# Performance work log

Measured on AMD Instinct MI355X. Metric: run time of the kernel, lower is better.

Reference implementation:

```python
import jax, jax.numpy as jnp
import numpy as np

B, N, C, H, D, K = 8, 2000, 64, 64, 16, 2  # batch, nodes, hidden, hidden_hidden, embed_dim, cheb_k


def setup_inputs() -> dict:
    key = jax.random.key(0)
    ks = jax.random.split(key, 12)
    f = lambda k, s, sc=1.0: jax.random.normal(k, s, dtype=jnp.float32) * sc
    return {
        "z": f(ks[0], (B, N, C)),
        "W_in": f(ks[1], (H, C), 0.1),
        "b_in": f(ks[2], (H,), 0.1),
        "W_out": f(ks[3], (C * C, H), 0.05),
        "b_out": f(ks[4], (C * C,), 0.05),
        "emb": f(ks[5], (N, D), 0.1),
        "wp": f(ks[6], (D, K, H, H), 0.1),
        "bp": f(ks[7], (D, H), 0.1),
        "w1": f(ks[8], (C,)),
        "w2": f(ks[9], (C,)),
        "vs": f(ks[10], (N, N), 0.02),
        "bs": f(ks[11], (N, N), 0.02),
    }


def reference(z, W_in, b_in, W_out, b_out, emb, wp, bp, w1, w2, vs, bs):
    # linear_in + relu: (B,N,C) -> (B,N,H)
    h = jax.nn.relu(jnp.einsum("bnc,hc->bnh", z, W_in) + b_in)

    # data-adaptive graph: softmax over rows of relu(emb @ emb^T)
    A = jax.nn.softmax(jax.nn.relu(emb @ emb.T), axis=1)  # (N,N)
    S = jnp.stack([jnp.eye(N, dtype=z.dtype), A], axis=0)  # (K,N,N), cheb_k=2

    # spatial attention on h (x = h.unsqueeze(1), f_in == H == C)
    e1 = h @ w1  # (B,N)
    e2 = h @ w2  # (B,N)
    prod = e1[:, :, None] * e2[:, None, :]  # (B,N,N) outer product
    E = jax.nn.softmax(
        jnp.einsum("nm,bmp->bnp", vs, jax.nn.sigmoid(prod + bs)), axis=-1
    )  # (B,N,N)

    # batched supports: E.unsqueeze(1) @ S -> (B,K,N,N)
    sup = jnp.einsum("bnm,kmp->bknp", E, S)

    # node-adaptive weights / bias
    weights = jnp.einsum("nd,dkio->nkio", emb, wp)  # (N,K,H,H)
    bias = emb @ bp  # (N,H)

    # graph conv
    x_g = jnp.einsum("bknm,bmc->bnkc", sup, h)  # (B,N,K,H)
    g = jnp.einsum("bnki,nkio->bno", x_g, weights) + bias  # (B,N,H)

    # linear_out + view + tanh, scaled by 0.1
    out = jnp.tanh(jnp.einsum("bnh,oh->bno", g, W_out) + b_out)
    return 0.1 * out.reshape(B, N, C, C)
```

## Files before the change

### kernel.cpp

```cpp
#include <hip/hip_runtime.h>
#include <hip/hip_bf16.h>

#define NN 2000
#define NP 2048
#define BB 8
#define HH 64
#define DD 16

typedef __hip_bfloat16 bf16;
typedef short bf16x8 __attribute__((ext_vector_type(8)));
typedef float f32x4 __attribute__((ext_vector_type(4)));

__device__ __forceinline__ float fast_sigmoid(float x) {
    return 1.0f / (1.0f + __expf(-x));
}
__device__ __forceinline__ float fast_tanh(float x) {
    float e = __expf(2.0f * x);
    return 1.0f - 2.0f / (e + 1.0f);
}

__device__ __forceinline__ void glds16(const void* g, void* l) {
    __builtin_amdgcn_global_load_lds(
        (const __attribute__((address_space(1))) void*)g,
        (__attribute__((address_space(3))) void*)l, 16, 0, 0);
}

__global__ __launch_bounds__(256) void k_h(
        const float* __restrict__ z, const float* __restrict__ W_in,
        const float* __restrict__ b_in, const float* __restrict__ w1,
        const float* __restrict__ w2, float* __restrict__ h,
        float* __restrict__ e1, float* __restrict__ e2) {
    __shared__ float WT[64 * 65];
    __shared__ float zs[4][64];
    int t = threadIdx.x;
    int lane = t & 63, ty = t >> 6;
    int bn0 = blockIdx.x * 4;
    for (int i = t; i < 64 * 64; i += 256) {
        int hh = i >> 6, c = i & 63;
        WT[c * 65 + hh] = W_in[i];
    }
    zs[ty][lane] = z[(size_t)(bn0 + ty) * 64 + lane];
    __syncthreads();
    float acc = b_in[lane];
    #pragma unroll
    for (int c = 0; c < 64; c++) acc += zs[ty][c] * WT[c * 65 + lane];
    float hv = fmaxf(acc, 0.0f);
    h[(size_t)(bn0 + ty) * 64 + lane] = hv;
    float p1 = hv * w1[lane], p2 = hv * w2[lane];
    #pragma unroll
    for (int off = 32; off > 0; off >>= 1) {
        p1 += __shfl_down(p1, off);
        p2 += __shfl_down(p2, off);
    }
    if (lane == 0) { e1[bn0 + ty] = p1; e2[bn0 + ty] = p2; }
}

__global__ __launch_bounds__(256) void k_A(const float* __restrict__ emb,
                                           bf16* __restrict__ A) {
    int i = blockIdx.x, t = threadIdx.x;
    if (i >= NN) {
        for (int j = t; j < NP; j += 256) A[(size_t)i * NP + j] = __float2bfloat16(0.0f);
        return;
    }
    __shared__ float ei[DD];
    __shared__ float rowbuf[NP];
    __shared__ float red[256];
    if (t < DD) ei[t] = emb[i * DD + t];
    __syncthreads();
    float lmax = -1e30f;
    for (int j = t; j < NP; j += 256) {
        float s = 0.0f;
        if (j < NN) {
            #pragma unroll
            for (int d = 0; d < DD; d++) s += ei[d] * emb[j * DD + d];
            s = fmaxf(s, 0.0f);
            lmax = fmaxf(lmax, s);
        }
        rowbuf[j] = s;
    }
    red[t] = lmax; __syncthreads();
    for (int o = 128; o > 0; o >>= 1) { if (t < o) red[t] = fmaxf(red[t], red[t + o]); __syncthreads(); }
    float mx = red[0];
    __syncthreads();
    float lsum = 0.0f;
    for (int j = t; j < NN; j += 256) {
        float e = __expf(rowbuf[j] - mx);
        rowbuf[j] = e; lsum += e;
    }
    red[t] = lsum; __syncthreads();
    for (int o = 128; o > 0; o >>= 1) { if (t < o) red[t] += red[t + o]; __syncthreads(); }
    float inv = 1.0f / red[0];
    for (int j = t; j < NP; j += 256)
        A[(size_t)i * NP + j] = __float2bfloat16(j < NN ? rowbuf[j] * inv : 0.0f);
}

__global__ __launch_bounds__(256) void k_misc(
        const float* __restrict__ vs, bf16* __restrict__ vs_bf,
        const float* __restrict__ W_out, bf16* __restrict__ Wo_bf,
        const float* __restrict__ emb, const float* __restrict__ wp,
        float* __restrict__ Wn_all) {
    __shared__ float embs[128 * 16];
    int bid = blockIdx.x, t = threadIdx.x;
    if (bid < 16384) {
        int id = bid * 256 + t;
        int n = id >> 11, m = id & (NP - 1);
        float v = (n < NN && m < NN) ? vs[n * NN + m] : 0.0f;
        vs_bf[id] = __float2bfloat16(v);
        return;
    }
    if (bid < 16384 + 1024) {
        int id = (bid - 16384) * 256 + t;
        Wo_bf[id] = __float2bfloat16(W_out[id]);
        return;
    }
    int wb = bid - 17408;
    int n0 = (wb & 15) * 128;
    int jo = (wb >> 4) * 256 + t;
    float wv[16];
    #pragma unroll
    for (int d = 0; d < 16; d++) wv[d] = wp[(size_t)d * 8192 + jo];
    for (int s = t; s < 128 * 16; s += 256) {
        int i = s >> 4, d = s & 15;
        int n = n0 + i;
        embs[s] = (n < NN) ? emb[n * 16 + d] : 0.f;
    }
    __syncthreads();
    for (int i = 0; i < 128; i++) {
        int n = n0 + i;
        if (n >= NN) break;
        const f32x4* ev = (const f32x4*)&embs[i * 16];
        f32x4 e0 = ev[0], e1 = ev[1], e2 = ev[2], e3 = ev[3];
        float a = 0.f;
        #pragma unroll
        for (int q = 0; q < 4; q++) a += e0[q] * wv[q];
        #pragma unroll
        for (int q = 0; q < 4; q++) a += e1[q] * wv[4 + q];
        #pragma unroll
        for (int q = 0; q < 4; q++) a += e2[q] * wv[8 + q];
        #pragma unroll
        for (int q = 0; q < 4; q++) a += e3[q] * wv[12 + q];
        Wn_all[(size_t)n * 8192 + jo] = a;
    }
}

__global__ __launch_bounds__(256) void k_hT(const float* __restrict__ h,
                                            bf16* __restrict__ hTcat,
                                            bf16* __restrict__ hsT) {
    __shared__ float tile[64 * 65];
    int nt = blockIdx.x, b = blockIdx.y;
    int tx = threadIdx.x & 63, ty = threadIdx.x >> 6;
    int n0 = nt * 64;
    for (int i = ty * 16; i < ty * 16 + 16; i++) {
        int n = n0 + i;
        tile[i * 65 + tx] = (n < NN) ? h[((size_t)b * NN + n) * 64 + tx] : 0.0f;
    }
    __syncthreads();
    for (int i = ty * 16; i < ty * 16 + 16; i++) {
        bf16 v = __float2bfloat16(tile[tx * 65 + i]);
        hTcat[((size_t)b * 64 + i) * NP + n0 + tx] = v;
        hsT[((size_t)b * 128 + i) * NP + n0 + tx] = v;
    }
}

__global__ __launch_bounds__(256) void k_AhT(const float* __restrict__ Ahcat,
                                             bf16* __restrict__ hsT) {
    __shared__ float tile[64 * 65];
    int pt = blockIdx.x, b = blockIdx.y;
    int tx = threadIdx.x & 63, ty = threadIdx.x >> 6;
    int p0 = pt * 64, q0 = b * 64;
    for (int i = ty * 16; i < ty * 16 + 16; i++)
        tile[i * 65 + tx] = Ahcat[((size_t)p0 + i) * 512 + q0 + tx];
    __syncthreads();
    for (int i = ty * 16; i < ty * 16 + 16; i++)
        hsT[((size_t)b * 128 + 64 + i) * NP + p0 + tx] =
            __float2bfloat16(tile[tx * 65 + i]);
}

__global__ __launch_bounds__(256) void k_Tt(const float* __restrict__ e1,
                                            const float* __restrict__ e2,
                                            const float* __restrict__ bs,
                                            bf16* __restrict__ Tt) {
    __shared__ float bst[64 * 65];
    __shared__ float tile[64 * 65];
    int mt = blockIdx.x, pt = blockIdx.y;
    int tx = threadIdx.x & 63, ty = threadIdx.x >> 6;
    int m0 = mt * 64, p0 = pt * 64;
    int p = p0 + tx;
    for (int i = ty * 16; i < ty * 16 + 16; i++) {
        int m = m0 + i;
        bst[i * 65 + tx] = (m < NN && p < NN) ? bs[(size_t)m * NN + p] : 0.0f;
    }
    __syncthreads();
    for (int b = 0; b < BB; b++) {
        float e2v = (p < NN) ? e2[b * NN + p] : 0.0f;
        for (int i = ty * 16; i < ty * 16 + 16; i++) {
            int m = m0 + i;
            float v = 0.0f;
            if (m < NN && p < NN)
                v = fast_sigmoid(e1[b * NN + m] * e2v + bst[i * 65 + tx]);
            tile[i * 65 + tx] = v;
        }
        __syncthreads();
        for (int i = ty * 16; i < ty * 16 + 16; i++)
            Tt[(size_t)b * NP * NP + ((size_t)p0 + i) * NP + m0 + tx] =
                __float2bfloat16(tile[tx * 65 + i]);
        __syncthreads();
    }
}

__global__ __launch_bounds__(512) void k_gemm256pv(
        const bf16* __restrict__ X, const bf16* __restrict__ Yt,
        const bf16* __restrict__ hsT, float* __restrict__ xgPart,
        float* __restrict__ rsPart,
        int K, int ldx, int ldy, long long sY, long long sHs) {
    __shared__ short LDSb[65536];
    short* Asb = LDSb;
    short* Bsb = LDSb + 32768;
    int id = blockIdx.x;
    int xcd = id & 7, jj0 = id >> 3;
    int member = jj0 & 7, glocal = jj0 >> 3;
    int group = glocal * 8 + xcd;
    int bx = member, by = group & 7, bz = group >> 3;
    int z = bz;
    const bf16* Xp = X;
    const bf16* Yp = Yt + (long long)z * sY;
    int tid = threadIdx.x;
    int m0 = bx * 256, n0 = by * 256;
    int wave = tid >> 6, lane = tid & 63;
    int wr = wave >> 2, wc = wave & 3;
    int fr = lane & 15, kq = lane >> 4;

    f32x4 zero = {0.f, 0.f, 0.f, 0.f};
    f32x4 acc[8][4];
    #pragma unroll
    for (int i = 0; i < 8; i++)
        #pragma unroll
        for (int j = 0; j < 4; j++) acc[i][j] = zero;

    int r8 = tid >> 3;
    int sslot = (tid & 7) ^ (r8 & 7);
    const bf16* xsrc = Xp + (long long)(m0 + r8) * ldx + sslot * 8;
    const bf16* ysrc = Yp + (long long)(n0 + r8) * ldy + sslot * 8;

    auto STAGE = [&](int tile) {
        short* Ab = Asb + (tile & 1) * 16384 + tid * 8;
        short* Bb = Bsb + (tile & 1) * 16384 + tid * 8;
        int ko = tile * 64;
        #pragma unroll
        for (int c = 0; c < 4; c++) {
            glds16(xsrc + (long long)(c * 64) * ldx + ko, Ab + c * 4096);
            glds16(ysrc + (long long)(c * 64) * ldy + ko, Bb + c * 4096);
        }
    };

    int NT = K >> 6;
    STAGE(0);
    STAGE(1);
    asm volatile("s_waitcnt vmcnt(8)" ::: "memory");
    __builtin_amdgcn_s_barrier();

    for (int t = 0; t < NT; t++) {
        const short* Ab = Asb + (t & 1) * 16384 + wr * 8192 + fr * 64;
        const short* Bb = Bsb + (t & 1) * 16384 + wc * 4096 + fr * 64;
        #pragma unroll
        for (int ks = 0; ks < 2; ks++) {
            int s = ((ks * 4 + kq) ^ (fr & 7)) * 8;
            bf16x8 a[8], b[4];
            #pragma unroll
            for (int i = 0; i < 8; i++)
                a[i] = *(const bf16x8*)(Ab + i * 1024 + s);
            #pragma unroll
            for (int j = 0; j < 4; j++)
                b[j] = *(const bf16x8*)(Bb + j * 1024 + s);
            __builtin_amdgcn_s_setprio(1);
            #pragma unroll
            for (int i = 0; i < 8; i++)
                #pragma unroll
                for (int j = 0; j < 4; j++)
                    acc[i][j] = __builtin_amdgcn_mfma_f32_16x16x32_bf16(a[i], b[j], acc[i][j], 0, 0, 0);
            __builtin_amdgcn_s_setprio(0);
        }
        __builtin_amdgcn_sched_barrier(0);
        __builtin_amdgcn_s_barrier();
        __builtin_amdgcn_sched_barrier(0);
        if (t + 2 < NT) {
            STAGE(t + 2);
            asm volatile("s_waitcnt vmcnt(8)" ::: "memory");
            __builtin_amdgcn_s_barrier();
        } else if (t + 1 < NT) {
            asm volatile("s_waitcnt vmcnt(0)" ::: "memory");
            __builtin_amdgcn_s_barrier();
        }
    }
    __syncthreads();

    int rq = kq * 4;
    #pragma unroll
    for (int i = 0; i < 8; i++) {
        #pragma unroll
        for (int r = 0; r < 4; r++) {
            int lrow = wr * 128 + i * 16 + rq + r;
            float rs = 0.f;
            #pragma unroll
            for (int j = 0; j < 4; j++) {
                int lcol = wc * 64 + j * 16 + fr;
                float e = (n0 + lcol < NN) ? __expf(acc[i][j][r]) : 0.f;
                bf16 bv = __float2bfloat16(e);
                int sl = (lcol >> 3) ^ (lrow & 7);
                LDSb[lrow * 256 + sl * 8 + (lcol & 7)] = *(short*)&bv;
                rs += e;
            }
            rs += __shfl_xor(rs, 1);
            rs += __shfl_xor(rs, 2);
            rs += __shfl_xor(rs, 4);
            rs += __shfl_xor(rs, 8);
            if (fr == 0)
                rsPart[((long long)z * 32 + by * 4 + wc) * NP + m0 + lrow] = rs;
        }
    }
    __syncthreads();

    const bf16* hz = hsT + (long long)z * sHs;
    int wr2 = wave >> 2, wc2 = wave & 3;
    f32x4 acc2[8][2];
    #pragma unroll
    for (int i = 0; i < 8; i++)
        #pragma unroll
        for (int jj = 0; jj < 2; jj++) acc2[i][jj] = zero;
    #pragma unroll
    for (int ks = 0; ks < 8; ks++) {
        bf16x8 a2[8], b2[2];
        #pragma unroll
        for (int i = 0; i < 8; i++) {
            int row = wr2 * 128 + i * 16 + fr;
            int sl = (ks * 4 + kq) ^ (row & 7);
            a2[i] = *(const bf16x8*)(LDSb + row * 256 + sl * 8);
        }
        #pragma unroll
        for (int jj = 0; jj < 2; jj++)
            b2[jj] = *(const bf16x8*)(hz + (long long)(wc2 * 32 + jj * 16 + fr) * NP
                                      + n0 + ks * 32 + kq * 8);
        #pragma unroll
        for (int i = 0; i < 8; i++)
            #pragma unroll
            for (int jj = 0; jj < 2; jj++)
                acc2[i][jj] = __builtin_amdgcn_mfma_f32_16x16x32_bf16(a2[i], b2[jj], acc2[i][jj], 0, 0, 0);
    }
    long long slab = (long long)by * ((long long)BB * NP * 128);
    #pragma unroll
    for (int i = 0; i < 8; i++)
        #pragma unroll
        for (int jj = 0; jj < 2; jj++) {
            int jcol = wc2 * 32 + jj * 16 + fr;
            #pragma unroll
            for (int r = 0; r < 4; r++) {
                int n = m0 + wr2 * 128 + i * 16 + rq + r;
                xgPart[slab + ((long long)z * NP + n) * 128 + jcol] = acc2[i][jj][r];
            }
        }
}

template<bool TANH, int KSPLIT>
__global__ __launch_bounds__(256) void k_gemm_bt(
        const bf16* __restrict__ X, const bf16* __restrict__ Yt,
        float* __restrict__ C, const float* __restrict__ bias,
        int K, int ldx, int ldy, int ldc,
        long long sX, long long sY, long long sC, long long sSlice) {
    __shared__ short As[128 * 32];
    __shared__ short Bs[128 * 32];
    int zz = blockIdx.z;
    int ks = 0;
    if (KSPLIT > 1) { ks = zz % KSPLIT; zz /= KSPLIT; }
    const bf16* Xp = X + (long long)zz * sX;
    const bf16* Yp = Yt + (long long)zz * sY;
    float* Cp = C + (long long)zz * sC + (long long)ks * sSlice;
    int tid = threadIdx.x;
    int m0 = blockIdx.x * 128, n0 = blockIdx.y * 128;
    int wave = tid >> 6, lane = tid & 63;
    int wm = (wave >> 1) * 64, wn = (wave & 1) * 64;
    int fr = lane & 15, kq = lane >> 4;

    f32x4 zero = {0.f, 0.f, 0.f, 0.f};
    f32x4 acc[4][4];
    #pragma unroll
    for (int i = 0; i < 4; i++)
        #pragma unroll
        for (int j = 0; j < 4; j++) acc[i][j] = zero;

    int lrow = lane >> 2, lcol = (lane & 3) * 8;
    const bf16* xg0 = Xp + (long long)(m0 + wave * 16 + lrow) * ldx + lcol;
    const bf16* xg1 = xg0 + (long long)64 * ldx;
    const bf16* yg0 = Yp + (long long)(n0 + wave * 16 + lrow) * ldy + lcol;
    const bf16* yg1 = yg0 + (long long)64 * ldy;
    short* lA0 = As + wave * 512;
    short* lA1 = As + (wave + 4) * 512;
    short* lB0 = Bs + wave * 512;
    short* lB1 = Bs + (wave + 4) * 512;

    int kbeg = (KSPLIT > 1) ? ks * (K / KSPLIT) : 0;
    int kend = kbeg + K / KSPLIT;
    for (int k0 = kbeg; k0 < kend; k0 += 32) {
        __syncthreads();
        glds16(xg0 + k0, lA0);
        glds16(xg1 + k0, lA1);
        glds16(yg0 + k0, lB0);
        glds16(yg1 + k0, lB1);
        __syncthreads();
        bf16x8 a[4], b[4];
        #pragma unroll
        for (int i = 0; i < 4; i++)
            a[i] = *(const bf16x8*)(As + (wm + i * 16 + fr) * 32 + kq * 8);
        #pragma unroll
        for (int j = 0; j < 4; j++)
            b[j] = *(const bf16x8*)(Bs + (wn + j * 16 + fr) * 32 + kq * 8);
        #pragma unroll
        for (int i = 0; i < 4; i++)
            #pragma unroll
            for (int j = 0; j < 4; j++)
                acc[i][j] = __builtin_amdgcn_mfma_f32_16x16x32_bf16(a[i], b[j], acc[i][j], 0, 0, 0);
    }
    int rq = kq * 4;
    for (int i = 0; i < 4; i++)
        for (int j = 0; j < 4; j++) {
            int col = n0 + wn + j * 16 + fr;
            float bv = TANH ? bias[col] : 0.0f;
            #pragma unroll
            for (int r = 0; r < 4; r++) {
                int row = m0 + wm + i * 16 + rq + r;
                float v = acc[i][j][r];
                Cp[(long long)row * ldc + col] =
                    TANH ? 0.1f * fast_tanh(v + bv) : v;
            }
        }
}

__global__ __launch_bounds__(256) void k_reduce8(const float* __restrict__ part,
                                                 float* __restrict__ out, int total) {
    int i = (blockIdx.x * 256 + threadIdx.x) * 4;
    f32x4 s = *(const f32x4*)(part + i);
    #pragma unroll
    for (int k = 1; k < 8; k++)
        s += *(const f32x4*)(part + (size_t)k * total + i);
    *(f32x4*)(out + i) = s;
}

__global__ __launch_bounds__(256) void k_g(
        const float* __restrict__ Wn_all, const float* __restrict__ bp,
        const float* __restrict__ emb, const float* __restrict__ xgPart,
        const float* __restrict__ rsPart, bf16* __restrict__ gbf) {
    __shared__ float Wn[8192];
    __shared__ float xgs[1024];
    __shared__ float biass[64];
    __shared__ float invs[8];
    const long long TOT = (long long)BB * NP * 128;
    int n = blockIdx.x, t = threadIdx.x;
    if (t < 8) {
        float s = 0.f;
        #pragma unroll
        for (int y = 0; y < 32; y++)
            s += rsPart[((size_t)t * 32 + y) * NP + n];
        invs[t] = 1.0f / s;
    }
    if (t >= 64 && t < 128) {
        int o = t - 64;
        float a = 0.f;
        #pragma unroll
        for (int d = 0; d < 16; d++) a += emb[n * 16 + d] * bp[d * 64 + o];
        biass[o] = a;
    }
    {
        const f32x4* src = (const f32x4*)(Wn_all + (size_t)n * 8192);
        f32x4* dst = (f32x4*)Wn;
        #pragma unroll
        for (int s = 0; s < 8; s++) dst[s * 256 + t] = src[s * 256 + t];
    }
    __syncthreads();
    for (int s = 0; s < 4; s++) {
        int id = t + s * 256;
        int b = id >> 7, j = id & 127;
        long long base = ((long long)b * NP + n) * 128 + j;
        float a = 0.f;
        #pragma unroll
        for (int sl = 0; sl < 8; sl++) a += xgPart[sl * TOT + base];
        xgs[id] = a * invs[b];
    }
    __syncthreads();
    int o = t & 63, bh = t >> 6;
    for (int half = 0; half < 2; half++) {
        int b = bh + half * 4;
        float a = biass[o];
        for (int j = 0; j < 128; j++) a += xgs[b * 128 + j] * Wn[j * 64 + o];
        gbf[((size_t)b * NN + n) * 64 + o] = __float2bfloat16(a);
    }
}

extern "C" void kernel_launch(void* const* d_in, const int* in_sizes, int n_in,
                              void* d_out, int out_size, void* d_ws, size_t ws_size,
                              hipStream_t stream) {
    const float* z     = (const float*)d_in[0];
    const float* W_in  = (const float*)d_in[1];
    const float* b_in  = (const float*)d_in[2];
    const float* W_out = (const float*)d_in[3];
    const float* b_out = (const float*)d_in[4];
    const float* emb   = (const float*)d_in[5];
    const float* wp    = (const float*)d_in[6];
    const float* bp    = (const float*)d_in[7];
    const float* w1    = (const float*)d_in[8];
    const float* w2    = (const float*)d_in[9];
    const float* vs    = (const float*)d_in[10];
    const float* bs    = (const float*)d_in[11];

    char* p = (char*)d_ws;
    auto alloc = [&](size_t bytes) -> char* {
        char* r = p;
        p += (bytes + 255) & ~(size_t)255;
        return r;
    };
    float* h       = (float*)alloc((size_t)BB * NN * 64 * 4);
    float* e1      = (float*)alloc((size_t)BB * NN * 4);
    float* e2      = (float*)alloc((size_t)BB * NN * 4);
    bf16*  A_bf    = (bf16*) alloc((size_t)NP * NP * 2);
    bf16*  vs_bf   = (bf16*) alloc((size_t)NP * NP * 2);
    bf16*  Tt_all  = (bf16*) alloc((size_t)BB * NP * NP * 2);
    float* rsPart  = (float*)alloc((size_t)BB * 32 * NP * 4);
    bf16*  hTcat   = (bf16*) alloc((size_t)512 * NP * 2);
    float* Ahcat   = (float*)alloc((size_t)NP * 512 * 4);
    float* AhPart  = (float*)alloc((size_t)8 * NP * 512 * 4);
    bf16*  hsT     = (bf16*) alloc((size_t)BB * 128 * NP * 2);
    float* xgPart8 = (float*)alloc((size_t)8 * BB * NP * 128 * 4);
    bf16*  gbf     = (bf16*) alloc((size_t)BB * NN * 64 * 2);
    bf16*  Wo_bf   = (bf16*) alloc((size_t)4096 * 64 * 2);
    float* Wn_all  = (float*)alloc((size_t)NN * 8192 * 4);

    k_h<<<BB * NN / 4, 256, 0, stream>>>(z, W_in, b_in, w1, w2, h, e1, e2);
    k_A<<<NP, 256, 0, stream>>>(emb, A_bf);
    k_misc<<<16384 + 1024 + 512, 256, 0, stream>>>(vs, vs_bf, W_out, Wo_bf,
                                                   emb, wp, Wn_all);
    k_hT<<<dim3(NP / 64, BB), 256, 0, stream>>>(h, hTcat, hsT);

    k_gemm_bt<false, 8><<<dim3(16, 4, 8), 256, 0, stream>>>(
        A_bf, hTcat, AhPart, nullptr, NP, NP, NP, 512,
        0, 0, 0, (long long)NP * 512);
    k_reduce8<<<(NP * 512) / 1024, 256, 0, stream>>>(AhPart, Ahcat, NP * 512);
    k_AhT<<<dim3(NP / 64, BB), 256, 0, stream>>>(Ahcat, hsT);

    k_Tt<<<dim3(NP / 64, NP / 64), 256, 0, stream>>>(e1, e2, bs, Tt_all);
    k_gemm256pv<<<512, 512, 0, stream>>>(
        vs_bf, Tt_all, hsT, xgPart8, rsPart, NP, NP, NP,
        (long long)NP * NP, (long long)128 * NP);

    k_g<<<NN, 256, 0, stream>>>(Wn_all, bp, emb, xgPart8, rsPart, gbf);
    k_gemm_bt<true, 1><<<dim3(125, 32, 1), 256, 0, stream>>>(
        gbf, Wo_bf, (float*)d_out, b_out, 64, 64, 64, 4096, 0, 0, 0, 0);
}
```

Baseline: 655.5 us.

## Deepen GEMM pipeline to four K32 stages, fuse reduce into transpose, parallelize Tt over batch

```diff
diff --git a/kernel.cpp b/kernel.cpp
--- a/kernel.cpp
+++ b/kernel.cpp
@@ -162,14 +162,20 @@
     }
 }
 
-__global__ __launch_bounds__(256) void k_AhT(const float* __restrict__ Ahcat,
-                                             bf16* __restrict__ hsT) {
+__global__ __launch_bounds__(256) void k_redT(const float* __restrict__ AhPart,
+                                              bf16* __restrict__ hsT) {
     __shared__ float tile[64 * 65];
     int pt = blockIdx.x, b = blockIdx.y;
     int tx = threadIdx.x & 63, ty = threadIdx.x >> 6;
     int p0 = pt * 64, q0 = b * 64;
-    for (int i = ty * 16; i < ty * 16 + 16; i++)
-        tile[i * 65 + tx] = Ahcat[((size_t)p0 + i) * 512 + q0 + tx];
+    const long long TOT = (long long)NP * 512;
+    for (int i = ty * 16; i < ty * 16 + 16; i++) {
+        long long base = ((long long)p0 + i) * 512 + q0 + tx;
+        float s = AhPart[base];
+        #pragma unroll
+        for (int sl = 1; sl < 8; sl++) s += AhPart[sl * TOT + base];
+        tile[i * 65 + tx] = s;
+    }
     __syncthreads();
     for (int i = ty * 16; i < ty * 16 + 16; i++)
         hsT[((size_t)b * 128 + 64 + i) * NP + p0 + tx] =
@@ -180,32 +186,26 @@
                                             const float* __restrict__ e2,
                                             const float* __restrict__ bs,
                                             bf16* __restrict__ Tt) {
-    __shared__ float bst[64 * 65];
     __shared__ float tile[64 * 65];
+    int b = blockIdx.z;
+    e1 += (size_t)b * NN;
+    e2 += (size_t)b * NN;
+    Tt += (size_t)b * NP * NP;
     int mt = blockIdx.x, pt = blockIdx.y;
     int tx = threadIdx.x & 63, ty = threadIdx.x >> 6;
     int m0 = mt * 64, p0 = pt * 64;
     int p = p0 + tx;
+    float e2v = (p < NN) ? e2[p] : 0.0f;
     for (int i = ty * 16; i < ty * 16 + 16; i++) {
         int m = m0 + i;
-        bst[i * 65 + tx] = (m < NN && p < NN) ? bs[(size_t)m * NN + p] : 0.0f;
-    }
-    __syncthreads();
-    for (int b = 0; b < BB; b++) {
-        float e2v = (p < NN) ? e2[b * NN + p] : 0.0f;
-        for (int i = ty * 16; i < ty * 16 + 16; i++) {
-            int m = m0 + i;
-            float v = 0.0f;
-            if (m < NN && p < NN)
-                v = fast_sigmoid(e1[b * NN + m] * e2v + bst[i * 65 + tx]);
-            tile[i * 65 + tx] = v;
-        }
-        __syncthreads();
-        for (int i = ty * 16; i < ty * 16 + 16; i++)
-            Tt[(size_t)b * NP * NP + ((size_t)p0 + i) * NP + m0 + tx] =
-                __float2bfloat16(tile[tx * 65 + i]);
-        __syncthreads();
-    }
+        float v = 0.0f;
+        if (m < NN && p < NN)
+            v = fast_sigmoid(e1[m] * e2v + bs[(size_t)m * NN + p]);
+        tile[i * 65 + tx] = v;
+    }
+    __syncthreads();
+    for (int i = ty * 16; i < ty * 16 + 16; i++)
+        Tt[((size_t)p0 + i) * NP + m0 + tx] = __float2bfloat16(tile[tx * 65 + i]);
 }
 
 __global__ __launch_bounds__(512) void k_gemm256pv(
@@ -237,60 +237,66 @@
         #pragma unroll
         for (int j = 0; j < 4; j++) acc[i][j] = zero;
 
-    int r8 = tid >> 3;
-    int sslot = (tid & 7) ^ (r8 & 7);
-    const bf16* xsrc = Xp + (long long)(m0 + r8) * ldx + sslot * 8;
-    const bf16* ysrc = Yp + (long long)(n0 + r8) * ldy + sslot * 8;
+    int r4 = tid >> 2, slot = tid & 3;
+    int scol = (slot ^ ((r4 >> 1) & 3)) * 8;
+    const bf16* xsrc = Xp + (long long)(m0 + r4) * ldx + scol;
+    const bf16* ysrc = Yp + (long long)(n0 + r4) * ldy + scol;
+    short* Ad = Asb + tid * 8;
+    short* Bd = Bsb + tid * 8;
 
     auto STAGE = [&](int tile) {
-        short* Ab = Asb + (tile & 1) * 16384 + tid * 8;
-        short* Bb = Bsb + (tile & 1) * 16384 + tid * 8;
-        int ko = tile * 64;
-        #pragma unroll
-        for (int c = 0; c < 4; c++) {
-            glds16(xsrc + (long long)(c * 64) * ldx + ko, Ab + c * 4096);
-            glds16(ysrc + (long long)(c * 64) * ldy + ko, Bb + c * 4096);
-        }
+        int buf = (tile & 3) * 8192;
+        long long ko = (long long)tile * 32;
+        glds16(xsrc + ko, Ad + buf);
+        glds16(xsrc + 128 * (long long)ldx + ko, Ad + buf + 4096);
+        glds16(ysrc + ko, Bd + buf);
+        glds16(ysrc + 128 * (long long)ldy + ko, Bd + buf + 4096);
     };
 
-    int NT = K >> 6;
-    STAGE(0);
-    STAGE(1);
+    int aoff[8], boff[4];
+    #pragma unroll
+    for (int i = 0; i < 8; i++) {
+        int row = wr * 128 + i * 16 + fr;
+        aoff[i] = row * 32 + ((kq ^ ((row >> 1) & 3)) << 3);
+    }
+    #pragma unroll
+    for (int j = 0; j < 4; j++) {
+        int row = wc * 64 + j * 16 + fr;
+        boff[j] = row * 32 + ((kq ^ ((row >> 1) & 3)) << 3);
+    }
+
+    int NT = K >> 5;
+    STAGE(0); STAGE(1); STAGE(2);
     asm volatile("s_waitcnt vmcnt(8)" ::: "memory");
     __builtin_amdgcn_s_barrier();
 
     for (int t = 0; t < NT; t++) {
-        const short* Ab = Asb + (t & 1) * 16384 + wr * 8192 + fr * 64;
-        const short* Bb = Bsb + (t & 1) * 16384 + wc * 4096 + fr * 64;
-        #pragma unroll
-        for (int ks = 0; ks < 2; ks++) {
-            int s = ((ks * 4 + kq) ^ (fr & 7)) * 8;
-            bf16x8 a[8], b[4];
-            #pragma unroll
-            for (int i = 0; i < 8; i++)
-                a[i] = *(const bf16x8*)(Ab + i * 1024 + s);
+        const short* Ab = Asb + (t & 3) * 8192;
+        const short* Bb = Bsb + (t & 3) * 8192;
+        bf16x8 a[8], b[4];
+        #pragma unroll
+        for (int i = 0; i < 8; i++) a[i] = *(const bf16x8*)(Ab + aoff[i]);
+        #pragma unroll
+        for (int j = 0; j < 4; j++) b[j] = *(const bf16x8*)(Bb + boff[j]);
+        __builtin_amdgcn_s_setprio(1);
+        #pragma unroll
+        for (int i = 0; i < 8; i++)
             #pragma unroll
             for (int j = 0; j < 4; j++)
-                b[j] = *(const bf16x8*)(Bb + j * 1024 + s);
-            __builtin_amdgcn_s_setprio(1);
-            #pragma unroll
-            for (int i = 0; i < 8; i++)
-                #pragma unroll
-                for (int j = 0; j < 4; j++)
-                    acc[i][j] = __builtin_amdgcn_mfma_f32_16x16x32_bf16(a[i], b[j], acc[i][j], 0, 0, 0);
-            __builtin_amdgcn_s_setprio(0);
-        }
+                acc[i][j] = __builtin_amdgcn_mfma_f32_16x16x32_bf16(a[i], b[j], acc[i][j], 0, 0, 0);
+        __builtin_amdgcn_s_setprio(0);
         __builtin_amdgcn_sched_barrier(0);
         __builtin_amdgcn_s_barrier();
         __builtin_amdgcn_sched_barrier(0);
-        if (t + 2 < NT) {
-            STAGE(t + 2);
+        if (t + 3 < NT) {
+            STAGE(t + 3);
             asm volatile("s_waitcnt vmcnt(8)" ::: "memory");
-            __builtin_amdgcn_s_barrier();
+        } else if (t + 2 < NT) {
+            asm volatile("s_waitcnt vmcnt(4)" ::: "memory");
         } else if (t + 1 < NT) {
             asm volatile("s_waitcnt vmcnt(0)" ::: "memory");
-            __builtin_amdgcn_s_barrier();
-        }
+        }
+        __builtin_amdgcn_s_barrier();
     }
     __syncthreads();
 
@@ -346,7 +352,6 @@
             for (int jj = 0; jj < 2; jj++)
                 acc2[i][jj] = __builtin_amdgcn_mfma_f32_16x16x32_bf16(a2[i], b2[jj], acc2[i][jj], 0, 0, 0);
     }
-    long long slab = (long long)by * ((long long)BB * NP * 128);
     #pragma unroll
     for (int i = 0; i < 8; i++)
         #pragma unroll
@@ -355,7 +360,7 @@
             #pragma unroll
             for (int r = 0; r < 4; r++) {
                 int n = m0 + wr2 * 128 + i * 16 + rq + r;
-                xgPart[slab + ((long long)z * NP + n) * 128 + jcol] = acc2[i][jj][r];
+                xgPart[(long long)n * 8192 + by * 1024 + z * 128 + jcol] = acc2[i][jj][r];
             }
         }
 }
@@ -434,25 +439,15 @@
         }
 }
 
-__global__ __launch_bounds__(256) void k_reduce8(const float* __restrict__ part,
-                                                 float* __restrict__ out, int total) {
-    int i = (blockIdx.x * 256 + threadIdx.x) * 4;
-    f32x4 s = *(const f32x4*)(part + i);
-    #pragma unroll
-    for (int k = 1; k < 8; k++)
-        s += *(const f32x4*)(part + (size_t)k * total + i);
-    *(f32x4*)(out + i) = s;
-}
-
 __global__ __launch_bounds__(256) void k_g(
         const float* __restrict__ Wn_all, const float* __restrict__ bp,
         const float* __restrict__ emb, const float* __restrict__ xgPart,
         const float* __restrict__ rsPart, bf16* __restrict__ gbf) {
     __shared__ float Wn[8192];
+    __shared__ float xgc[8192];
     __shared__ float xgs[1024];
     __shared__ float biass[64];
     __shared__ float invs[8];
-    const long long TOT = (long long)BB * NP * 128;
     int n = blockIdx.x, t = threadIdx.x;
     if (t < 8) {
         float s = 0.f;
@@ -470,18 +465,22 @@
     }
     {
         const f32x4* src = (const f32x4*)(Wn_all + (size_t)n * 8192);
+        const f32x4* xsrc = (const f32x4*)(xgPart + (size_t)n * 8192);
         f32x4* dst = (f32x4*)Wn;
-        #pragma unroll
-        for (int s = 0; s < 8; s++) dst[s * 256 + t] = src[s * 256 + t];
+        f32x4* xdst = (f32x4*)xgc;
+        #pragma unroll
+        for (int s = 0; s < 8; s++) {
+            dst[s * 256 + t] = src[s * 256 + t];
+            xdst[s * 256 + t] = xsrc[s * 256 + t];
+        }
     }
     __syncthreads();
     for (int s = 0; s < 4; s++) {
         int id = t + s * 256;
         int b = id >> 7, j = id & 127;
-        long long base = ((long long)b * NP + n) * 128 + j;
-        float a = 0.f;
-        #pragma unroll
-        for (int sl = 0; sl < 8; sl++) a += xgPart[sl * TOT + base];
+        float a = xgc[b * 128 + j];
+        #pragma unroll
+        for (int by = 1; by < 8; by++) a += xgc[by * 1024 + b * 128 + j];
         xgs[id] = a * invs[b];
     }
     __syncthreads();
@@ -524,10 +523,9 @@
     bf16*  Tt_all  = (bf16*) alloc((size_t)BB * NP * NP * 2);
     float* rsPart  = (float*)alloc((size_t)BB * 32 * NP * 4);
     bf16*  hTcat   = (bf16*) alloc((size_t)512 * NP * 2);
-    float* Ahcat   = (float*)alloc((size_t)NP * 512 * 4);
     float* AhPart  = (float*)alloc((size_t)8 * NP * 512 * 4);
     bf16*  hsT     = (bf16*) alloc((size_t)BB * 128 * NP * 2);
-    float* xgPart8 = (float*)alloc((size_t)8 * BB * NP * 128 * 4);
+    float* xgPart  = (float*)alloc((size_t)NP * 8192 * 4);
     bf16*  gbf     = (bf16*) alloc((size_t)BB * NN * 64 * 2);
     bf16*  Wo_bf   = (bf16*) alloc((size_t)4096 * 64 * 2);
     float* Wn_all  = (float*)alloc((size_t)NN * 8192 * 4);
@@ -541,15 +539,14 @@
     k_gemm_bt<false, 8><<<dim3(16, 4, 8), 256, 0, stream>>>(
         A_bf, hTcat, AhPart, nullptr, NP, NP, NP, 512,
         0, 0, 0, (long long)NP * 512);
-    k_reduce8<<<(NP * 512) / 1024, 256, 0, stream>>>(AhPart, Ahcat, NP * 512);
-    k_AhT<<<dim3(NP / 64, BB), 256, 0, stream>>>(Ahcat, hsT);
-
-    k_Tt<<<dim3(NP / 64, NP / 64), 256, 0, stream>>>(e1, e2, bs, Tt_all);
+    k_redT<<<dim3(NP / 64, BB), 256, 0, stream>>>(AhPart, hsT);
+
+    k_Tt<<<dim3(NP / 64, NP / 64, BB), 256, 0, stream>>>(e1, e2, bs, Tt_all);
     k_gemm256pv<<<512, 512, 0, stream>>>(
-        vs_bf, Tt_all, hsT, xgPart8, rsPart, NP, NP, NP,
+        vs_bf, Tt_all, hsT, xgPart, rsPart, NP, NP, NP,
         (long long)NP * NP, (long long)128 * NP);
 
-    k_g<<<NN, 256, 0, stream>>>(Wn_all, bp, emb, xgPart8, rsPart, gbf);
+    k_g<<<NN, 256, 0, stream>>>(Wn_all, bp, emb, xgPart, rsPart, gbf);
     k_gemm_bt<true, 1><<<dim3(125, 32, 1), 256, 0, stream>>>(
         gbf, Wo_bf, (float*)d_out, b_out, 64, 64, 64, 4096, 0, 0, 0, 0);
 }
```

Result: no change. 650.5 us (-0.8%).
